# Kernel optimization log

Measured on AMD Instinct MI355X. Metric: run time of the kernel, lower is better.

## Reference

```python
import jax, jax.numpy as jnp
import numpy as np

NU, NM, H, E, EL, L = 100000, 20000, 64, 1000000, 500000, 3
BN_EPS = 1e-5


def setup_inputs() -> dict:
    key = jax.random.key(0)
    ks = jax.random.split(key, 16)
    f = lambda k, s: jax.random.normal(k, s, jnp.float32) * 0.05
    return {
        "n_id": jnp.arange(NU, dtype=jnp.int32),
        "movie_x": f(ks[0], (NM, H)),
        "edge_user": jax.random.randint(ks[1], (E,), 0, NU, dtype=jnp.int32),
        "edge_movie": jax.random.randint(ks[2], (E,), 0, NM, dtype=jnp.int32),
        "label_user": jax.random.randint(ks[3], (EL,), 0, NU, dtype=jnp.int32),
        "label_movie": jax.random.randint(ks[4], (EL,), 0, NM, dtype=jnp.int32),
        "user_emb": f(ks[5], (NU, H)),
        "Wl_um": f(ks[6], (L, H, H)), "b_um": jnp.zeros((L, H), jnp.float32), "Wr_um": f(ks[7], (L, H, H)),
        "Wl_mu": f(ks[8], (L, H, H)), "b_mu": jnp.zeros((L, H), jnp.float32), "Wr_mu": f(ks[9], (L, H, H)),
        "proj_u_W": f(ks[10], (L * H, H)), "proj_u_b": jnp.zeros((H,), jnp.float32),
        "proj_m_W": f(ks[11], (L * H, H)), "proj_m_b": jnp.zeros((H,), jnp.float32),
        "W1": f(ks[12], (2 * H, H)), "b1": jnp.zeros((H,), jnp.float32),
        "g1": jnp.ones((H,), jnp.float32), "be1": jnp.zeros((H,), jnp.float32),
        "W2": f(ks[13], (H, H // 2)), "b2": jnp.zeros((H // 2,), jnp.float32),
        "g2": jnp.ones((H // 2,), jnp.float32), "be2": jnp.zeros((H // 2,), jnp.float32),
        "W3": f(ks[14], (H // 2, 1)), "b3": jnp.zeros((1,), jnp.float32),
    }


def _sage(x_src, x_dst, src_idx, dst_idx, Wl, b, Wr, num_dst):
    # PyG SAGEConv: lin_l(mean_agg of neighbor feats) + lin_r(root feats)
    msg = x_src[src_idx]                                   # [E, d_src] gather
    s = jax.ops.segment_sum(msg, dst_idx, num_segments=num_dst)
    cnt = jax.ops.segment_sum(jnp.ones((src_idx.shape[0],), x_src.dtype), dst_idx, num_segments=num_dst)
    agg = s / jnp.maximum(cnt, 1.0)[:, None]               # mean aggregation
    return agg @ Wl + b + x_dst @ Wr


def _bn(x, gamma, beta):
    m = jnp.mean(x, axis=0)
    v = jnp.var(x, axis=0)  # biased, as torch BN training-mode normalization
    return gamma * (x - m) * jax.lax.rsqrt(v + BN_EPS) + beta


def reference(n_id, movie_x, edge_user, edge_movie, label_user, label_movie, user_emb,
              Wl_um, b_um, Wr_um, Wl_mu, b_mu, Wr_mu,
              proj_u_W, proj_u_b, proj_m_W, proj_m_b,
              W1, b1, g1, be1, W2, b2, g2, be2, W3, b3):
    x_u = user_emb[n_id]          # embedding lookup
    x_m = movie_x
    outs_u, outs_m = [], []
    for i in range(L):
        # both hetero convs read the same input x_dict (to_hetero semantics)
        new_m = _sage(x_u, x_m, edge_user, edge_movie, Wl_um[i], b_um[i], Wr_um[i], NM)
        new_u = _sage(x_m, x_u, edge_movie, edge_user, Wl_mu[i], b_mu[i], Wr_mu[i], NU)
        x_m = jax.nn.relu(new_m)
        x_u = jax.nn.relu(new_u)
        outs_m.append(x_m)
        outs_u.append(x_u)
    # JumpingKnowledge 'cat' + per-node-type output projection
    h_u = jnp.concatenate(outs_u, axis=-1) @ proj_u_W + proj_u_b   # [NU, H]
    h_m = jnp.concatenate(outs_m, axis=-1) @ proj_m_W + proj_m_b   # [NM, H]
    # edge classifier
    combined = jnp.concatenate([h_u[label_user], h_m[label_movie]], axis=-1)  # [EL, 2H]
    z = jax.nn.relu(_bn(combined @ W1 + b1, g1, be1))
    z = jax.nn.relu(_bn(z @ W2 + b2, g2, be2))
    return (z @ W3 + b3)[:, 0]
```

## Files before the change

kernel.cpp:

```cpp
#include <hip/hip_runtime.h>


namespace {

typedef unsigned int u32;
typedef unsigned short ushort_t;
typedef __attribute__((ext_vector_type(8))) short bfrag;
typedef __attribute__((ext_vector_type(4))) float f32x4;

constexpr int NUc = 100000;
constexpr int NMc = 20000;
constexpr int HD  = 64;
constexpr int NE  = 1000000;
constexpr int ELc = 500000;
constexpr int NL  = 3;
constexpr float BN_EPS = 1e-5f;

constexpr int CAPU = 48;
constexpr int CAPM = 112;
constexpr int NPASS = 8;

constexpr int PREP_BLOCKS = 6 * 24 + 16 + 4;
constexpr int STATS_BLOCKS = 512;

__device__ __forceinline__ float bflo(u32 u) { return __uint_as_float(u << 16); }
__device__ __forceinline__ float bfhi(u32 u) { return __uint_as_float(u & 0xffff0000u); }
__device__ __forceinline__ u32 rbf(float f) {
  u32 u = __float_as_uint(f);
  return (u + 0x7fffu + ((u >> 16) & 1u)) >> 16;
}
__device__ __forceinline__ u32 packbf(float lo, float hi) { return rbf(lo) | (rbf(hi) << 16); }

__device__ __forceinline__ f32x4 mfma16(bfrag a, bfrag b, f32x4 c) {
  return __builtin_amdgcn_mfma_f32_16x16x32_bf16(a, b, c, 0, 0, 0);
}


__global__ void scatter_pass_kernel(const int* __restrict__ eu, const int* __restrict__ em,
                                    int* __restrict__ cu, int* __restrict__ cm,
                                    int* __restrict__ su, int* __restrict__ sm,
                                    int ulo, int uhi, int mlo, int mhi) {
  int t4 = (blockIdx.x * 256 + threadIdx.x) * 4;
  if (t4 < NE) {
    int4 u4 = *(const int4*)(eu + t4);
    int4 m4 = *(const int4*)(em + t4);
#pragma unroll
    for (int j = 0; j < 4; j++) {
      int u = (j == 0) ? u4.x : (j == 1) ? u4.y : (j == 2) ? u4.z : u4.w;
      int m = (j == 0) ? m4.x : (j == 1) ? m4.y : (j == 2) ? m4.z : m4.w;
      if (u >= ulo && u < uhi) {
        int p = atomicAdd(&cu[u], 1);
        if (p < CAPU) su[(size_t)u * CAPU + p] = m;
      }
      if (m >= mlo && m < mhi) {
        int p = atomicAdd(&cm[m], 1);
        if (p < CAPM) sm[(size_t)m * CAPM + p] = u;
      }
    }
  }
}

__global__ void gatherconv_kernel(const int* __restrict__ n_id, const float* __restrict__ emb,
                                  u32* __restrict__ xu0,
                                  const float* __restrict__ mx, u32* __restrict__ xm0) {
  int t = blockIdx.x * 256 + threadIdx.x;
  if (t < NUc * 8) {
    int n = t >> 3, c = t & 7;
    const float* src = emb + (size_t)n_id[n] * HD + c * 8;
    float4 a = *(const float4*)src, b = *(const float4*)(src + 4);
    *(uint4*)(xu0 + (size_t)n * 32 + c * 4) =
        make_uint4(packbf(a.x, a.y), packbf(a.z, a.w), packbf(b.x, b.y), packbf(b.z, b.w));
  } else if (t < NUc * 8 + NMc * 8) {
    int tt = t - NUc * 8;
    int n = tt >> 3, c = tt & 7;
    const float* src = mx + (size_t)n * HD + c * 8;
    float4 a = *(const float4*)src, b = *(const float4*)(src + 4);
    *(uint4*)(xm0 + (size_t)n * 32 + c * 4) =
        make_uint4(packbf(a.x, a.y), packbf(a.z, a.w), packbf(b.x, b.y), packbf(b.z, b.w));
  }
}


__global__ void aggregate_fused_kernel(const int* __restrict__ cnt_m, const int* __restrict__ sm,
                                       const u32* __restrict__ xu, int xu_s,
                                       u32* __restrict__ agg_m,
                                       const int* __restrict__ cnt_u, const int* __restrict__ su,
                                       const u32* __restrict__ xm, int xm_s,
                                       u32* __restrict__ agg_u) {
  int gid  = blockIdx.x * 256 + threadIdx.x;
  int w    = gid >> 6;
  int lane = gid & 63;
  if (w >= NMc + NUc) return;
  const int* src;
  const u32* table;
  u32* outp;
  int stride, deg;
  size_t base;
  if (w < NMc) {
    deg = min(cnt_m[w], CAPM);
    base = (size_t)w * CAPM;
    src = sm; table = xu; stride = xu_s;
    outp = agg_m + (size_t)w * 32;
  } else {
    int wu = w - NMc;
    deg = min(cnt_u[wu], CAPU);
    base = (size_t)wu * CAPU;
    src = su; table = xm; stride = xm_s;
    outp = agg_u + (size_t)wu * 32;
  }
  int f4 = lane & 7;
  int es = lane >> 3;
  float a0 = 0.f, a1 = 0.f, a2 = 0.f, a3 = 0.f;
  float a4 = 0.f, a5 = 0.f, a6 = 0.f, a7 = 0.f;
  int nfull = deg & ~15;
  int i = 0;
  for (; i < nfull; i += 16) {
    int e0 = src[base + i + es];
    int e1 = src[base + i + 8 + es];
    uint4 v0 = *(const uint4*)(table + (size_t)e0 * stride + 4 * f4);
    uint4 v1 = *(const uint4*)(table + (size_t)e1 * stride + 4 * f4);
    a0 += bflo(v0.x) + bflo(v1.x);
    a1 += bfhi(v0.x) + bfhi(v1.x);
    a2 += bflo(v0.y) + bflo(v1.y);
    a3 += bfhi(v0.y) + bfhi(v1.y);
    a4 += bflo(v0.z) + bflo(v1.z);
    a5 += bfhi(v0.z) + bfhi(v1.z);
    a6 += bflo(v0.w) + bflo(v1.w);
    a7 += bfhi(v0.w) + bfhi(v1.w);
  }
  for (; i < deg; i += 8) {
    int e = i + es;
    if (e < deg) {
      uint4 v = *(const uint4*)(table + (size_t)src[base + e] * stride + 4 * f4);
      a0 += bflo(v.x); a1 += bfhi(v.x);
      a2 += bflo(v.y); a3 += bfhi(v.y);
      a4 += bflo(v.z); a5 += bfhi(v.z);
      a6 += bflo(v.w); a7 += bfhi(v.w);
    }
  }
#pragma unroll
  for (int mask = 8; mask < 64; mask <<= 1) {
    a0 += __shfl_xor(a0, mask); a1 += __shfl_xor(a1, mask);
    a2 += __shfl_xor(a2, mask); a3 += __shfl_xor(a3, mask);
    a4 += __shfl_xor(a4, mask); a5 += __shfl_xor(a5, mask);
    a6 += __shfl_xor(a6, mask); a7 += __shfl_xor(a7, mask);
  }
  float inv = 1.f / fmaxf((float)deg, 1.f);
  if (es == 0) {
    uint4 o;
    o.x = packbf(a0 * inv, a1 * inv);
    o.y = packbf(a2 * inv, a3 * inv);
    o.z = packbf(a4 * inv, a5 * inv);
    o.w = packbf(a6 * inv, a7 * inv);
    *(uint4*)(outp + 4 * f4) = o;
  }
}


struct PrepArgs {
  const float* src[8];
  u32* hi[8];
  u32* lo[8];
  int nblk[8];
};

__global__ __launch_bounds__(64) void prep_all_kernel(PrepArgs args) {
  int b = blockIdx.x;
  int e = 0;
  while (e < 8 && b >= args.nblk[e]) { b -= args.nblk[e]; e++; }
  if (e >= 8) return;
  int l = threadIdx.x;
  u32 hi[4], lo[4];
  if (e < 7) {
    int m = b >> 3, s = (b >> 2) & 1, c = b & 3;
    int n  = c * 16 + (l & 15);
    int k0 = s * 32 + (l >> 4) * 8;
    const float* src = args.src[e] + (size_t)m * 4096;
#pragma unroll
    for (int p = 0; p < 4; p++) {
      float v0 = src[(k0 + 2 * p) * 64 + n];
      float v1 = src[(k0 + 2 * p + 1) * 64 + n];
      u32 h0 = rbf(v0), h1 = rbf(v1);
      float r0 = v0 - __uint_as_float(h0 << 16);
      float r1 = v1 - __uint_as_float(h1 << 16);
      hi[p] = h0 | (h1 << 16);
      lo[p] = rbf(r0) | (rbf(r1) << 16);
    }
    *(uint4*)(args.hi[e] + ((size_t)b * 64 + l) * 4) = make_uint4(hi[0], hi[1], hi[2], hi[3]);
    *(uint4*)(args.lo[e] + ((size_t)b * 64 + l) * 4) = make_uint4(lo[0], lo[1], lo[2], lo[3]);
  } else {
    int s = b >> 1, c = b & 1;
    int n  = c * 16 + (l & 15);
    int k0 = s * 32 + (l >> 4) * 8;
    const float* src = args.src[7];
#pragma unroll
    for (int p = 0; p < 4; p++) {
      float v0 = src[(k0 + 2 * p) * 32 + n];
      float v1 = src[(k0 + 2 * p + 1) * 32 + n];
      u32 h0 = rbf(v0), h1 = rbf(v1);
      float r0 = v0 - __uint_as_float(h0 << 16);
      float r1 = v1 - __uint_as_float(h1 << 16);
      hi[p] = h0 | (h1 << 16);
      lo[p] = rbf(r0) | (rbf(r1) << 16);
    }
    *(uint4*)(args.hi[7] + ((size_t)b * 64 + l) * 4) = make_uint4(hi[0], hi[1], hi[2], hi[3]);
    *(uint4*)(args.lo[7] + ((size_t)b * 64 + l) * 4) = make_uint4(lo[0], lo[1], lo[2], lo[3]);
  }
}

__device__ __forceinline__ size_t foff(int ks, int c, int l) {
  return ((size_t)((ks * 4 + c) * 64 + l)) * 4;
}
__device__ __forceinline__ size_t foff32(int s, int c, int l) {
  return ((size_t)((s * 2 + c) * 64 + l)) * 4;
}


__global__ __launch_bounds__(256) void sage_fused_kernel(
    int tm, int tu,
    const u32* __restrict__ agg_m, const u32* __restrict__ xm_prev, int sm_s,
    const u32* __restrict__ whiLm, const u32* __restrict__ wloLm,
    const u32* __restrict__ whiRm, const u32* __restrict__ wloRm,
    const float* __restrict__ bias_m, u32* __restrict__ out_m,
    const u32* __restrict__ agg_u, const u32* __restrict__ xu_prev, int su_s,
    const u32* __restrict__ whiLu, const u32* __restrict__ wloLu,
    const u32* __restrict__ whiRu, const u32* __restrict__ wloRu,
    const float* __restrict__ bias_u, u32* __restrict__ out_u) {
  int tile = blockIdx.x * 4 + (threadIdx.x >> 6);
  if (tile >= tm + tu) return;
  int lane = threadIdx.x & 63;
  const u32 *agg, *xin, *whiL, *wloL, *whiR, *wloR;
  const float* bias;
  u32* out;
  int xs;
  if (tile < tm) {
    agg = agg_m; xin = xm_prev; xs = sm_s;
    whiL = whiLm; wloL = wloLm; whiR = whiRm; wloR = wloRm;
    bias = bias_m; out = out_m;
  } else {
    tile -= tm;
    agg = agg_u; xin = xu_prev; xs = su_s;
    whiL = whiLu; wloL = wloLu; whiR = whiRu; wloR = wloRu;
    bias = bias_u; out = out_u;
  }
  int r  = tile * 16 + (lane & 15);
  int kq = lane >> 4;
  f32x4 acc[4];
#pragma unroll
  for (int c = 0; c < 4; c++) acc[c] = (f32x4){0.f, 0.f, 0.f, 0.f};
  const u32* arow0 = agg + (size_t)r * 32 + kq * 4;
  const u32* arow1 = xin + (size_t)r * xs + kq * 4;
#pragma unroll
  for (int s = 0; s < 2; s++) {
    bfrag a = *(const bfrag*)(arow0 + s * 16);
#pragma unroll
    for (int c = 0; c < 4; c++) {
      bfrag bh = *(const bfrag*)(whiL + foff(s, c, lane));
      bfrag bl = *(const bfrag*)(wloL + foff(s, c, lane));
      acc[c] = mfma16(a, bh, acc[c]);
      acc[c] = mfma16(a, bl, acc[c]);
    }
  }
#pragma unroll
  for (int s = 0; s < 2; s++) {
    bfrag a = *(const bfrag*)(arow1 + s * 16);
#pragma unroll
    for (int c = 0; c < 4; c++) {
      bfrag bh = *(const bfrag*)(whiR + foff(s, c, lane));
      bfrag bl = *(const bfrag*)(wloR + foff(s, c, lane));
      acc[c] = mfma16(a, bh, acc[c]);
      acc[c] = mfma16(a, bl, acc[c]);
    }
  }
  ushort_t* ob = (ushort_t*)out;
  int rowb = tile * 16 + (lane >> 4) * 4;
  int col0 = lane & 15;
#pragma unroll
  for (int c = 0; c < 4; c++) {
    float bb = bias[c * 16 + col0];
#pragma unroll
    for (int g = 0; g < 4; g++) {
      float v = fmaxf(acc[c][g] + bb, 0.f);
      ob[(size_t)(rowb + g) * 192 + c * 16 + col0] = (ushort_t)rbf(v);
    }
  }
}

__global__ __launch_bounds__(256) void proj_fused_kernel(
    int tu, int tm,
    const u32* __restrict__ xin_u, const u32* __restrict__ whi_u, const u32* __restrict__ wlo_u,
    const float* __restrict__ bias_u, u32* __restrict__ out_u,
    const u32* __restrict__ xin_m, const u32* __restrict__ whi_m, const u32* __restrict__ wlo_m,
    const float* __restrict__ bias_m, u32* __restrict__ out_m) {
  int tile = blockIdx.x * 4 + (threadIdx.x >> 6);
  if (tile >= tu + tm) return;
  int lane = threadIdx.x & 63;
  const u32 *xin, *whi, *wlo;
  const float* bias;
  u32* out;
  if (tile < tu) {
    xin = xin_u; whi = whi_u; wlo = wlo_u; bias = bias_u; out = out_u;
  } else {
    tile -= tu;
    xin = xin_m; whi = whi_m; wlo = wlo_m; bias = bias_m; out = out_m;
  }
  int r  = tile * 16 + (lane & 15);
  int kq = lane >> 4;
  f32x4 acc[4];
#pragma unroll
  for (int c = 0; c < 4; c++) acc[c] = (f32x4){0.f, 0.f, 0.f, 0.f};
  const u32* arow = xin + (size_t)r * 96 + kq * 4;
#pragma unroll
  for (int ks = 0; ks < 6; ks++) {
    bfrag a = *(const bfrag*)(arow + ks * 16);
#pragma unroll
    for (int c = 0; c < 4; c++) {
      bfrag bh = *(const bfrag*)(whi + foff(ks, c, lane));
      bfrag bl = *(const bfrag*)(wlo + foff(ks, c, lane));
      acc[c] = mfma16(a, bh, acc[c]);
      acc[c] = mfma16(a, bl, acc[c]);
    }
  }
  ushort_t* ob = (ushort_t*)out;
  int rowb = tile * 16 + (lane >> 4) * 4;
  int col0 = lane & 15;
#pragma unroll
  for (int c = 0; c < 4; c++) {
    float bb = bias[c * 16 + col0];
#pragma unroll
    for (int g = 0; g < 4; g++) {
      float v = acc[c][g] + bb;
      ob[(size_t)(rowb + g) * 64 + c * 16 + col0] = (ushort_t)rbf(v);
    }
  }
}

__global__ __launch_bounds__(256) void cls1_mfma_kernel(
    int ntiles, const u32* __restrict__ hu, const u32* __restrict__ hm,
    const int* __restrict__ lu, const int* __restrict__ lm,
    const u32* __restrict__ whi, const u32* __restrict__ wlo,
    const float* __restrict__ b1, u32* __restrict__ y1) {
  int wid = blockIdx.x * 4 + (threadIdx.x >> 6);
  int t0 = wid * 2;
  if (t0 >= ntiles) return;
  int lane = threadIdx.x & 63;
  int rit = lane & 15;
  int kq  = lane >> 4;
  int r0 = t0 * 16 + rit;
  int r1 = r0 + 16;
  int gu0 = lu[r0], gm0 = lm[r0];
  int gu1 = lu[r1], gm1 = lm[r1];
  f32x4 acc0[4], acc1[4];
#pragma unroll
  for (int c = 0; c < 4; c++) {
    acc0[c] = (f32x4){0.f, 0.f, 0.f, 0.f};
    acc1[c] = (f32x4){0.f, 0.f, 0.f, 0.f};
  }
  const u32* pu0 = hu + (size_t)gu0 * 32 + kq * 4;
  const u32* pm0 = hm + (size_t)gm0 * 32 + kq * 4;
  const u32* pu1 = hu + (size_t)gu1 * 32 + kq * 4;
  const u32* pm1 = hm + (size_t)gm1 * 32 + kq * 4;
#pragma unroll
  for (int s = 0; s < 2; s++) {
    bfrag au0 = *(const bfrag*)(pu0 + s * 16);
    bfrag au1 = *(const bfrag*)(pu1 + s * 16);
#pragma unroll
    for (int c = 0; c < 4; c++) {
      bfrag bh = *(const bfrag*)(whi + foff(s, c, lane));
      bfrag bl = *(const bfrag*)(wlo + foff(s, c, lane));
      acc0[c] = mfma16(au0, bh, acc0[c]);
      acc0[c] = mfma16(au0, bl, acc0[c]);
      acc1[c] = mfma16(au1, bh, acc1[c]);
      acc1[c] = mfma16(au1, bl, acc1[c]);
    }
  }
#pragma unroll
  for (int s = 0; s < 2; s++) {
    bfrag am0 = *(const bfrag*)(pm0 + s * 16);
    bfrag am1 = *(const bfrag*)(pm1 + s * 16);
#pragma unroll
    for (int c = 0; c < 4; c++) {
      bfrag bh = *(const bfrag*)(whi + foff(2 + s, c, lane));
      bfrag bl = *(const bfrag*)(wlo + foff(2 + s, c, lane));
      acc0[c] = mfma16(am0, bh, acc0[c]);
      acc0[c] = mfma16(am0, bl, acc0[c]);
      acc1[c] = mfma16(am1, bh, acc1[c]);
      acc1[c] = mfma16(am1, bl, acc1[c]);
    }
  }
  ushort_t* ob = (ushort_t*)y1;
  int col0 = lane & 15;
  int rowb0 = t0 * 16 + kq * 4;
  int rowb1 = rowb0 + 16;
#pragma unroll
  for (int c = 0; c < 4; c++) {
    float bb = b1[c * 16 + col0];
#pragma unroll
    for (int g = 0; g < 4; g++) {
      float v0 = acc0[c][g] + bb;
      float v1 = acc1[c][g] + bb;
      ob[(size_t)(rowb0 + g) * 64 + c * 16 + col0] = (ushort_t)rbf(v0);
      ob[(size_t)(rowb1 + g) * 64 + c * 16 + col0] = (ushort_t)rbf(v1);
    }
  }
}

__global__ __launch_bounds__(256) void cls2_mfma_kernel(
    int ntiles, const u32* __restrict__ y1,
    const float* __restrict__ scale1, const float* __restrict__ shift1,
    const u32* __restrict__ whi, const u32* __restrict__ wlo,
    const float* __restrict__ b2, u32* __restrict__ y2) {
  int tile = blockIdx.x * 4 + (threadIdx.x >> 6);
  if (tile >= ntiles) return;
  int lane = threadIdx.x & 63;
  int r  = tile * 16 + (lane & 15);
  int kq = lane >> 4;
  f32x4 acc[2];
  acc[0] = (f32x4){0.f, 0.f, 0.f, 0.f};
  acc[1] = (f32x4){0.f, 0.f, 0.f, 0.f};
  const u32* xrow = y1 + (size_t)r * 32 + kq * 4;
#pragma unroll
  for (int s = 0; s < 2; s++) {
    uint4 q = *(const uint4*)(xrow + s * 16);
    int kb = s * 32 + kq * 8;
    float a0 = fmaxf(bflo(q.x) * scale1[kb + 0] + shift1[kb + 0], 0.f);
    float a1 = fmaxf(bfhi(q.x) * scale1[kb + 1] + shift1[kb + 1], 0.f);
    float a2 = fmaxf(bflo(q.y) * scale1[kb + 2] + shift1[kb + 2], 0.f);
    float a3 = fmaxf(bfhi(q.y) * scale1[kb + 3] + shift1[kb + 3], 0.f);
    float a4 = fmaxf(bflo(q.z) * scale1[kb + 4] + shift1[kb + 4], 0.f);
    float a5 = fmaxf(bfhi(q.z) * scale1[kb + 5] + shift1[kb + 5], 0.f);
    float a6 = fmaxf(bflo(q.w) * scale1[kb + 6] + shift1[kb + 6], 0.f);
    float a7 = fmaxf(bfhi(q.w) * scale1[kb + 7] + shift1[kb + 7], 0.f);
    uint4 pa = make_uint4(packbf(a0, a1), packbf(a2, a3), packbf(a4, a5), packbf(a6, a7));
    bfrag a = *(bfrag*)&pa;
#pragma unroll
    for (int c = 0; c < 2; c++) {
      bfrag bh = *(const bfrag*)(whi + foff32(s, c, lane));
      bfrag bl = *(const bfrag*)(wlo + foff32(s, c, lane));
      acc[c] = mfma16(a, bh, acc[c]);
      acc[c] = mfma16(a, bl, acc[c]);
    }
  }
  ushort_t* ob = (ushort_t*)y2;
  int rowb = tile * 16 + (lane >> 4) * 4;
  int col0 = lane & 15;
#pragma unroll
  for (int c = 0; c < 2; c++) {
    float bb = b2[c * 16 + col0];
#pragma unroll
    for (int g = 0; g < 4; g++) {
      float v = acc[c][g] + bb;
      ob[(size_t)(rowb + g) * 32 + c * 16 + col0] = (ushort_t)rbf(v);
    }
  }
}


template <int CU>
__global__ __launch_bounds__(256) void stats_fast_kernel(const u32* __restrict__ y, int nrows,
                                                         float* __restrict__ sum,
                                                         float* __restrict__ ssq) {
  constexpr int TPR = CU / 4;
  constexpr int RPI = 256 / TPR;
  int t = threadIdx.x;
  int q  = t % TPR;
  int rg = t / TPR;
  float4 sA = {0.f, 0.f, 0.f, 0.f}, sB = {0.f, 0.f, 0.f, 0.f};
  float4 qA = {0.f, 0.f, 0.f, 0.f}, qB = {0.f, 0.f, 0.f, 0.f};
  for (int row = blockIdx.x * RPI + rg; row < nrows; row += gridDim.x * RPI) {
    uint4 v = *(const uint4*)(y + (size_t)row * CU + q * 4);
    float a0 = bflo(v.x), a1 = bfhi(v.x), a2 = bflo(v.y), a3 = bfhi(v.y);
    float a4 = bflo(v.z), a5 = bfhi(v.z), a6 = bflo(v.w), a7 = bfhi(v.w);
    sA.x += a0; qA.x += a0 * a0;
    sA.y += a1; qA.y += a1 * a1;
    sA.z += a2; qA.z += a2 * a2;
    sA.w += a3; qA.w += a3 * a3;
    sB.x += a4; qB.x += a4 * a4;
    sB.y += a5; qB.y += a5 * a5;
    sB.z += a6; qB.z += a6 * a6;
    sB.w += a7; qB.w += a7 * a7;
  }
#pragma unroll
  for (int mask = TPR; mask < 64; mask <<= 1) {
    sA.x += __shfl_xor(sA.x, mask); sA.y += __shfl_xor(sA.y, mask);
    sA.z += __shfl_xor(sA.z, mask); sA.w += __shfl_xor(sA.w, mask);
    sB.x += __shfl_xor(sB.x, mask); sB.y += __shfl_xor(sB.y, mask);
    sB.z += __shfl_xor(sB.z, mask); sB.w += __shfl_xor(sB.w, mask);
    qA.x += __shfl_xor(qA.x, mask); qA.y += __shfl_xor(qA.y, mask);
    qA.z += __shfl_xor(qA.z, mask); qA.w += __shfl_xor(qA.w, mask);
    qB.x += __shfl_xor(qB.x, mask); qB.y += __shfl_xor(qB.y, mask);
    qB.z += __shfl_xor(qB.z, mask); qB.w += __shfl_xor(qB.w, mask);
  }
  __shared__ float part[4][TPR][16];
  int wv = t >> 6, lane = t & 63;
  if (lane < TPR) {
    float* p = part[wv][lane];
    p[0] = sA.x; p[1] = sA.y; p[2] = sA.z; p[3] = sA.w;
    p[4] = sB.x; p[5] = sB.y; p[6] = sB.z; p[7] = sB.w;
    p[8] = qA.x; p[9] = qA.y; p[10] = qA.z; p[11] = qA.w;
    p[12] = qB.x; p[13] = qB.y; p[14] = qB.z; p[15] = qB.w;
  }
  __syncthreads();
  if (t < TPR * 16) {
    int qq = t >> 4, j = t & 15;
    float v = part[0][qq][j] + part[1][qq][j] + part[2][qq][j] + part[3][qq][j];
    if (j < 8) atomicAdd(&sum[qq * 8 + j], v);
    else       atomicAdd(&ssq[qq * 8 + (j - 8)], v);
  }
}

__global__ void bn_finalize_kernel(const float* __restrict__ sum, const float* __restrict__ ssq,
                                   const float* __restrict__ g, const float* __restrict__ be,
                                   int ncols, float inv_n,
                                   float* __restrict__ scale, float* __restrict__ shift) {
  int t = threadIdx.x;
  if (t < ncols) {
    float m = sum[t] * inv_n;
    float v = ssq[t] * inv_n - m * m;
    float rstd = rsqrtf(v + BN_EPS);
    float sc = g[t] * rstd;
    scale[t] = sc;
    shift[t] = be[t] - m * sc;
  }
}

__global__ void cls3_kernel(const u32* __restrict__ y2, const float* __restrict__ scale2,
                            const float* __restrict__ shift2, const float* __restrict__ W3,
                            const float* __restrict__ b3, float* __restrict__ outp) {
  int r = blockIdx.x * 256 + threadIdx.x;
  if (r >= ELc) return;
  const u32* yr = y2 + (size_t)r * 16;
  float s = b3[0];
#pragma unroll
  for (int j = 0; j < 16; j++) {
    u32 u = yr[j];
    float v0 = fmaxf(bflo(u) * scale2[2 * j] + shift2[2 * j], 0.f);
    float v1 = fmaxf(bfhi(u) * scale2[2 * j + 1] + shift2[2 * j + 1], 0.f);
    s += v0 * W3[2 * j] + v1 * W3[2 * j + 1];
  }
  outp[r] = s;
}

}

extern "C" void kernel_launch(void* const* d_in, const int* in_sizes, int n_in,
                              void* d_out, int out_size, void* d_ws, size_t ws_size,
                              hipStream_t stream) {
  const int*   n_id    = (const int*)d_in[0];
  const float* movie_x = (const float*)d_in[1];
  const int*   eu      = (const int*)d_in[2];
  const int*   em      = (const int*)d_in[3];
  const int*   lu      = (const int*)d_in[4];
  const int*   lm      = (const int*)d_in[5];
  const float* uemb    = (const float*)d_in[6];
  const float* Wl_um   = (const float*)d_in[7];
  const float* b_um    = (const float*)d_in[8];
  const float* Wr_um   = (const float*)d_in[9];
  const float* Wl_mu   = (const float*)d_in[10];
  const float* b_mu    = (const float*)d_in[11];
  const float* Wr_mu   = (const float*)d_in[12];
  const float* puW     = (const float*)d_in[13];
  const float* pub     = (const float*)d_in[14];
  const float* pmW     = (const float*)d_in[15];
  const float* pmb     = (const float*)d_in[16];
  const float* W1      = (const float*)d_in[17];
  const float* b1      = (const float*)d_in[18];
  const float* g1      = (const float*)d_in[19];
  const float* be1     = (const float*)d_in[20];
  const float* W2      = (const float*)d_in[21];
  const float* b2      = (const float*)d_in[22];
  const float* g2      = (const float*)d_in[23];
  const float* be2     = (const float*)d_in[24];
  const float* W3      = (const float*)d_in[25];
  const float* b3      = (const float*)d_in[26];
  float* outp = (float*)d_out;

  u32* ws = (u32*)d_ws;
  size_t o = 0;
  u32* xu0    = ws + o; o += (size_t)NUc * 32;
  u32* xm0    = ws + o; o += (size_t)NMc * 32;
  u32* outs_u = ws + o; o += (size_t)NUc * 96;
  u32* outs_m = ws + o; o += (size_t)NMc * 96;
  u32* agg_u  = ws + o; o += (size_t)NUc * 32;
  u32* agg_m  = ws + o; o += (size_t)NMc * 32;
  u32* y1 = ws;
  u32* y2     = ws + o; o += (size_t)ELc * 16;
  u32* h_u    = ws + o; o += (size_t)NUc * 32;
  u32* h_m    = ws + o; o += (size_t)NMc * 32;
  int* su     = (int*)(ws + o); o += (size_t)NUc * CAPU;
  int* sm     = (int*)(ws + o); o += (size_t)NMc * CAPM;
  int* cnt_u  = (int*)(ws + o); o += NUc;
  int* cnt_m  = (int*)(ws + o); o += NMc;
  float* stats = (float*)(ws + o); o += 512;
  u32* frWlum_h = ws + o; o += 3 * 2048;  u32* frWlum_l = ws + o; o += 3 * 2048;
  u32* frWrum_h = ws + o; o += 3 * 2048;  u32* frWrum_l = ws + o; o += 3 * 2048;
  u32* frWlmu_h = ws + o; o += 3 * 2048;  u32* frWlmu_l = ws + o; o += 3 * 2048;
  u32* frWrmu_h = ws + o; o += 3 * 2048;  u32* frWrmu_l = ws + o; o += 3 * 2048;
  u32* frPu_h   = ws + o; o += 3 * 2048;  u32* frPu_l   = ws + o; o += 3 * 2048;
  u32* frPm_h   = ws + o; o += 3 * 2048;  u32* frPm_l   = ws + o; o += 3 * 2048;
  u32* frW1_h   = ws + o; o += 2 * 2048;  u32* frW1_l   = ws + o; o += 2 * 2048;
  u32* frW2_h   = ws + o; o += 1024;      u32* frW2_l   = ws + o; o += 1024;
  if (ws_size < o * sizeof(u32)) return;

  float* sum1 = stats,        *ssq1 = stats + 64;
  float* sum2 = stats + 128,  *ssq2 = stats + 160;
  float* scale1 = stats + 192, *shift1 = stats + 256;
  float* scale2 = stats + 320, *shift2 = stats + 352;

  hipMemsetAsync(cnt_u, 0, (NUc + NMc + 192) * sizeof(int), stream);

  PrepArgs pa;
  pa.src[0] = Wl_um; pa.hi[0] = frWlum_h; pa.lo[0] = frWlum_l; pa.nblk[0] = 24;
  pa.src[1] = Wr_um; pa.hi[1] = frWrum_h; pa.lo[1] = frWrum_l; pa.nblk[1] = 24;
  pa.src[2] = Wl_mu; pa.hi[2] = frWlmu_h; pa.lo[2] = frWlmu_l; pa.nblk[2] = 24;
  pa.src[3] = Wr_mu; pa.hi[3] = frWrmu_h; pa.lo[3] = frWrmu_l; pa.nblk[3] = 24;
  pa.src[4] = puW;   pa.hi[4] = frPu_h;   pa.lo[4] = frPu_l;   pa.nblk[4] = 24;
  pa.src[5] = pmW;   pa.hi[5] = frPm_h;   pa.lo[5] = frPm_l;   pa.nblk[5] = 24;
  pa.src[6] = W1;    pa.hi[6] = frW1_h;   pa.lo[6] = frW1_l;   pa.nblk[6] = 16;
  pa.src[7] = W2;    pa.hi[7] = frW2_h;   pa.lo[7] = frW2_l;   pa.nblk[7] = 4;
  prep_all_kernel<<<PREP_BLOCKS, 64, 0, stream>>>(pa);

  int eb4 = (NE / 4 + 255) / 256;
  for (int p = 0; p < NPASS; p++) {
    scatter_pass_kernel<<<eb4, 256, 0, stream>>>(
        eu, em, cnt_u, cnt_m, su, sm,
        p * (NUc / NPASS), (p + 1) * (NUc / NPASS),
        p * (NMc / NPASS), (p + 1) * (NMc / NPASS));
  }
  gatherconv_kernel<<<((NUc + NMc) * 8 + 255) / 256, 256, 0, stream>>>(
      n_id, uemb, xu0, movie_x, xm0);

  int tu = NUc / 16, tm = NMc / 16;
  int agg_grid = ((NMc + NUc) * 64 + 255) / 256;
  for (int i = 0; i < NL; i++) {
    const u32* xu_prev = (i == 0) ? xu0 : (outs_u + (size_t)(i - 1) * 32);
    const u32* xm_prev = (i == 0) ? xm0 : (outs_m + (size_t)(i - 1) * 32);
    int su_s = (i == 0) ? 32 : 96;
    int sm_s = (i == 0) ? 32 : 96;
    aggregate_fused_kernel<<<agg_grid, 256, 0, stream>>>(
        cnt_m, sm, xu_prev, su_s, agg_m,
        cnt_u, su, xm_prev, sm_s, agg_u);
    sage_fused_kernel<<<(tm + tu + 3) / 4, 256, 0, stream>>>(
        tm, tu,
        agg_m, xm_prev, sm_s,
        frWlum_h + (size_t)i * 2048, frWlum_l + (size_t)i * 2048,
        frWrum_h + (size_t)i * 2048, frWrum_l + (size_t)i * 2048,
        b_um + (size_t)i * HD, outs_m + (size_t)i * 32,
        agg_u, xu_prev, su_s,
        frWlmu_h + (size_t)i * 2048, frWlmu_l + (size_t)i * 2048,
        frWrmu_h + (size_t)i * 2048, frWrmu_l + (size_t)i * 2048,
        b_mu + (size_t)i * HD, outs_u + (size_t)i * 32);
  }

  proj_fused_kernel<<<(tu + tm + 3) / 4, 256, 0, stream>>>(
      tu, tm, outs_u, frPu_h, frPu_l, pub, h_u,
      outs_m, frPm_h, frPm_l, pmb, h_m);

  int tl = ELc / 16;
  cls1_mfma_kernel<<<(tl / 2 + 3) / 4, 256, 0, stream>>>(tl, h_u, h_m, lu, lm, frW1_h, frW1_l, b1, y1);
  stats_fast_kernel<32><<<STATS_BLOCKS, 256, 0, stream>>>(y1, ELc, sum1, ssq1);
  bn_finalize_kernel<<<1, 64, 0, stream>>>(sum1, ssq1, g1, be1, 64, 1.f / ELc, scale1, shift1);
  cls2_mfma_kernel<<<(tl + 3) / 4, 256, 0, stream>>>(tl, y1, scale1, shift1, frW2_h, frW2_l, b2, y2);
  stats_fast_kernel<16><<<STATS_BLOCKS, 256, 0, stream>>>(y2, ELc, sum2, ssq2);
  bn_finalize_kernel<<<1, 64, 0, stream>>>(sum2, ssq2, g2, be2, 32, 1.f / ELc, scale2, shift2);
  cls3_kernel<<<(ELc + 255) / 256, 256, 0, stream>>>(y2, scale2, shift2, W3, b3, outp);
}
```

Before: 559.9 us.

## Split movie-side aggregation into source-range sweeps and halve scatter passes

Movie-node aggregation now reads its neighbour list four times, each pass gathering only user rows within one quarter of the user-id range. The aim is to keep the active slice of the user feature table cache-resident across concurrently running waves. The user-side path keeps its original unrolled loop, and the scatter pass count drops from 8 to 4. In exchange, index reads and branch checks grow fourfold and the two-edge unroll on the movie side is lost.

```diff
diff --git a/kernel.cpp b/kernel.cpp
--- a/kernel.cpp
+++ b/kernel.cpp
@@ -18,7 +18,8 @@
 
 constexpr int CAPU = 48;
 constexpr int CAPM = 112;
-constexpr int NPASS = 8;
+constexpr int NPASS = 4;
+constexpr int ASP = 4;
 
 constexpr int PREP_BLOCKS = 6 * 24 + 16 + 4;
 constexpr int STATS_BLOCKS = 512;
@@ -91,51 +92,63 @@
   int w    = gid >> 6;
   int lane = gid & 63;
   if (w >= NMc + NUc) return;
-  const int* src;
-  const u32* table;
-  u32* outp;
-  int stride, deg;
-  size_t base;
-  if (w < NMc) {
-    deg = min(cnt_m[w], CAPM);
-    base = (size_t)w * CAPM;
-    src = sm; table = xu; stride = xu_s;
-    outp = agg_m + (size_t)w * 32;
-  } else {
-    int wu = w - NMc;
-    deg = min(cnt_u[wu], CAPU);
-    base = (size_t)wu * CAPU;
-    src = su; table = xm; stride = xm_s;
-    outp = agg_u + (size_t)wu * 32;
-  }
   int f4 = lane & 7;
   int es = lane >> 3;
   float a0 = 0.f, a1 = 0.f, a2 = 0.f, a3 = 0.f;
   float a4 = 0.f, a5 = 0.f, a6 = 0.f, a7 = 0.f;
-  int nfull = deg & ~15;
-  int i = 0;
-  for (; i < nfull; i += 16) {
-    int e0 = src[base + i + es];
-    int e1 = src[base + i + 8 + es];
-    uint4 v0 = *(const uint4*)(table + (size_t)e0 * stride + 4 * f4);
-    uint4 v1 = *(const uint4*)(table + (size_t)e1 * stride + 4 * f4);
-    a0 += bflo(v0.x) + bflo(v1.x);
-    a1 += bfhi(v0.x) + bfhi(v1.x);
-    a2 += bflo(v0.y) + bflo(v1.y);
-    a3 += bfhi(v0.y) + bfhi(v1.y);
-    a4 += bflo(v0.z) + bflo(v1.z);
-    a5 += bfhi(v0.z) + bfhi(v1.z);
-    a6 += bflo(v0.w) + bflo(v1.w);
-    a7 += bfhi(v0.w) + bfhi(v1.w);
-  }
-  for (; i < deg; i += 8) {
-    int e = i + es;
-    if (e < deg) {
-      uint4 v = *(const uint4*)(table + (size_t)src[base + e] * stride + 4 * f4);
-      a0 += bflo(v.x); a1 += bfhi(v.x);
-      a2 += bflo(v.y); a3 += bfhi(v.y);
-      a4 += bflo(v.z); a5 += bfhi(v.z);
-      a6 += bflo(v.w); a7 += bfhi(v.w);
+  u32* outp;
+  int deg;
+  if (w < NMc) {
+    deg = min(cnt_m[w], CAPM);
+    size_t base = (size_t)w * CAPM;
+    outp = agg_m + (size_t)w * 32;
+#pragma unroll
+    for (int sp = 0; sp < ASP; sp++) {
+      int lo = sp * (NUc / ASP), hi = lo + (NUc / ASP);
+      for (int i = 0; i < deg; i += 8) {
+        int e = i + es;
+        if (e < deg) {
+          int s = sm[base + e];
+          if (s >= lo && s < hi) {
+            uint4 v = *(const uint4*)(xu + (size_t)s * xu_s + 4 * f4);
+            a0 += bflo(v.x); a1 += bfhi(v.x);
+            a2 += bflo(v.y); a3 += bfhi(v.y);
+            a4 += bflo(v.z); a5 += bfhi(v.z);
+            a6 += bflo(v.w); a7 += bfhi(v.w);
+          }
+        }
+      }
+    }
+  } else {
+    int wu = w - NMc;
+    deg = min(cnt_u[wu], CAPU);
+    size_t base = (size_t)wu * CAPU;
+    outp = agg_u + (size_t)wu * 32;
+    int nfull = deg & ~15;
+    int i = 0;
+    for (; i < nfull; i += 16) {
+      int e0 = su[base + i + es];
+      int e1 = su[base + i + 8 + es];
+      uint4 v0 = *(const uint4*)(xm + (size_t)e0 * xm_s + 4 * f4);
+      uint4 v1 = *(const uint4*)(xm + (size_t)e1 * xm_s + 4 * f4);
+      a0 += bflo(v0.x) + bflo(v1.x);
+      a1 += bfhi(v0.x) + bfhi(v1.x);
+      a2 += bflo(v0.y) + bflo(v1.y);
+      a3 += bfhi(v0.y) + bfhi(v1.y);
+      a4 += bflo(v0.z) + bflo(v1.z);
+      a5 += bfhi(v0.z) + bfhi(v1.z);
+      a6 += bflo(v0.w) + bflo(v1.w);
+      a7 += bfhi(v0.w) + bfhi(v1.w);
+    }
+    for (; i < deg; i += 8) {
+      int e = i + es;
+      if (e < deg) {
+        uint4 v = *(const uint4*)(xm + (size_t)su[base + e] * xm_s + 4 * f4);
+        a0 += bflo(v.x); a1 += bfhi(v.x);
+        a2 += bflo(v.y); a3 += bfhi(v.y);
+        a4 += bflo(v.z); a5 += bfhi(v.z);
+        a6 += bflo(v.w); a7 += bfhi(v.w);
+      }
     }
   }
 #pragma unroll
```

Result: slower. 585.7 us (+4.6%).
